# Kernel optimization log

Measured on AMD Instinct MI355X. Metric: run time of the kernel, lower is better.

The kernel has to match this reference:

```python
import jax, jax.numpy as jnp
import numpy as np

B, L, D, H, NE, M, NP, C, F2 = 2, 1024, 768, 12, 42, 8, 1722, 97, 256


def setup_inputs() -> dict:
    key = jax.random.key(0)
    ks = jax.random.split(key, 12)
    s = 0.02
    sequence_output = jax.random.normal(ks[0], (B, L, D), jnp.float32)
    attention = jax.random.uniform(ks[1], (B, H, L, L), jnp.float32)
    mention_idx = jax.random.randint(ks[2], (B, NE, M), 0, L)
    mention_mask = jax.random.randint(ks[3], (B, NE, M), 0, 2).at[:, :, 0].set(1)
    hts = jax.random.randint(ks[4], (B, NP, 2), 0, NE)
    return dict(
        sequence_output=sequence_output, attention=attention,
        mention_idx=mention_idx, mention_mask=mention_mask, hts=hts,
        W_lin=jax.random.normal(ks[5], (D, 3)) * s, b_lin=jnp.zeros((3,)),
        W_seg=jax.random.normal(ks[6], (3, F2)) * s, b_seg=jnp.zeros((F2,)),
        W_head=jax.random.normal(ks[7], (D, F2)) * s, b_head=jnp.zeros((F2,)),
        W_tail=jax.random.normal(ks[8], (D, F2)) * s, b_tail=jnp.zeros((F2,)),
        W_bil=jax.random.normal(ks[9], (C, F2, F2)) * s, b_bil=jnp.zeros((C,)),
    )


def reference(sequence_output, attention, mention_idx, mention_mask, hts,
              W_lin, b_lin, W_seg, b_seg, W_head, b_head, W_tail, b_tail,
              W_bil, b_bil):
    b_, l_, d_ = sequence_output.shape
    h_ = attention.shape[1]
    ne, m_ = mention_idx.shape[1:]
    NEG = jnp.asarray(-1e30, sequence_output.dtype)
    msk = mention_mask.astype(sequence_output.dtype)  # [B,NE,M]

    bidx = jnp.arange(b_)[:, None, None]
    # --- get_hrt: per-entity mention gather + logsumexp pool / mean pool ---
    ment_emb = sequence_output[bidx, mention_idx]              # [B,NE,M,D]
    ent_emb = jax.nn.logsumexp(jnp.where(msk[..., None] > 0, ment_emb, NEG), axis=2)  # [B,NE,D]
    ment_att = attention[bidx, :, mention_idx]                 # [B,NE,M,H,L]
    ent_att = (ment_att * msk[..., None, None]).sum(2) / msk.sum(2)[..., None, None]  # [B,NE,H,L]

    b2 = jnp.arange(b_)[:, None]
    hs = ent_emb[b2, hts[..., 0]]                              # [B,NP,D]
    ts = ent_emb[b2, hts[..., 1]]

    # --- get_channel_map: all ne*ne pair attention-weighted context ---
    hi = jnp.repeat(jnp.arange(ne), ne)
    ti = jnp.tile(jnp.arange(ne), ne)
    h_att = ent_att[:, hi]                                     # [B,NE*NE,H,L]
    t_att = ent_att[:, ti]
    ht_att = jnp.einsum('bphl,bphl->bpl', h_att, t_att) / h_   # mean over heads
    ht_att = ht_att / (ht_att.sum(-1, keepdims=True) + 1e-5)
    rs = jnp.einsum('bld,bpl->bpd', sequence_output, ht_att)   # [B,NE*NE,D]
    feature_map = rs.reshape(b_, ne, ne, d_)

    # self.linear (D->3) then segmentation net (stand-in: 1x1 conv 3->F2 + relu)
    attn_input = feature_map @ W_lin + b_lin                   # [B,NE,NE,3]
    attn_map = jax.nn.relu(attn_input @ W_seg + b_seg)         # [B,NE,NE,F2]

    # --- get_ht: gather pair features ---
    h_t = attn_map[b2, hts[..., 0], hts[..., 1]]               # [B,NP,F2]
    hs = jnp.tanh(hs @ W_head + b_head + h_t)
    ts = jnp.tanh(ts @ W_tail + b_tail + h_t)
    logits = jnp.einsum('bpi,oij,bpj->bpo', hs, W_bil, ts) + b_bil
    return logits.reshape(-1, logits.shape[-1])               # [B*NP, C]
```

## Files before the change

### kernel.cpp

```cpp
#include <hip/hip_runtime.h>
#include <hip/hip_bf16.h>
#include <math.h>

constexpr int BB = 2;
constexpr int LL = 1024;
constexpr int DD = 768;
constexpr int HH = 12;
constexpr int NEz = 42;
constexpr int MM = 8;
constexpr int NPp = 1722;
constexpr int CC = 97;
constexpr int FF = 256;
constexpr int PAIRS = NEz * NEz;
constexpr int TOTAL = BB * NPp;

constexpr int MT = 96;
constexpr int NT = 36;
constexpr int OG2 = 7;
constexpr int NOG = 14;
constexpr int NWG2 = NT * NOG;

typedef float f32x4 __attribute__((ext_vector_type(4)));
typedef short bf16x8 __attribute__((ext_vector_type(8)));
typedef unsigned short u16x4 __attribute__((ext_vector_type(4)));

__device__ inline short f2bs(float x) {
    __hip_bfloat16 b = __float2bfloat16(x);
    return *(short*)&b;
}
__device__ inline float bs2f(unsigned short u) {
    return __uint_as_float(((unsigned)u) << 16);
}
__device__ inline void gload16(const void* g, void* l) {
    __builtin_amdgcn_global_load_lds((const __attribute__((address_space(1))) unsigned int*)g,
                                     (__attribute__((address_space(3))) unsigned int*)l, 16, 0, 0);
}

__global__ void k_seqw(const float* __restrict__ seq, const float* __restrict__ Wl,
                       float* __restrict__ seqW) {
    int bl = blockIdx.x;
    int lane = threadIdx.x;
    const float* row = seq + (size_t)bl * DD;
    float a0 = 0.f, a1 = 0.f, a2 = 0.f;
    for (int d = lane; d < DD; d += 64) {
        float v = row[d];
        a0 += v * Wl[d * 3 + 0];
        a1 += v * Wl[d * 3 + 1];
        a2 += v * Wl[d * 3 + 2];
    }
    for (int off = 32; off; off >>= 1) {
        a0 += __shfl_down(a0, off);
        a1 += __shfl_down(a1, off);
        a2 += __shfl_down(a2, off);
    }
    if (lane == 0) {
        seqW[bl * 3 + 0] = a0;
        seqW[bl * 3 + 1] = a1;
        seqW[bl * 3 + 2] = a2;
    }
}

__global__ void k_ent_emb(const float* __restrict__ seq, const int* __restrict__ midx,
                          const int* __restrict__ mmask, float* __restrict__ ent_emb) {
    int be = blockIdx.x;
    int b = be / NEz;
    int tid = threadIdx.x;
    int idx[MM], msk[MM];
#pragma unroll
    for (int m = 0; m < MM; ++m) {
        idx[m] = midx[be * MM + m];
        msk[m] = mmask[be * MM + m];
    }
    const float* sb = seq + (size_t)b * LL * DD;
    for (int d = tid; d < DD; d += 256) {
        float v[MM];
        float mx = -1e30f;
#pragma unroll
        for (int m = 0; m < MM; ++m) {
            v[m] = msk[m] ? sb[(size_t)idx[m] * DD + d] : -1e30f;
            mx = fmaxf(mx, v[m]);
        }
        float s = 0.f;
#pragma unroll
        for (int m = 0; m < MM; ++m) s += expf(v[m] - mx);
        ent_emb[(size_t)be * DD + d] = mx + logf(s);
    }
}

__global__ void k_ent_att(const float* __restrict__ att, const int* __restrict__ midx,
                          const int* __restrict__ mmask, float* __restrict__ ea) {
    int beh = blockIdx.x;
    int h = beh % HH;
    int be = beh / HH;
    int b = be / NEz;
    int tid = threadIdx.x;
    int idx[MM], msk[MM];
    float msum = 0.f;
#pragma unroll
    for (int m = 0; m < MM; ++m) {
        idx[m] = midx[be * MM + m];
        msk[m] = mmask[be * MM + m];
        msum += (float)msk[m];
    }
    float inv = 1.f / msum;
    const float* ab = att + ((size_t)b * HH + h) * LL * LL;
#pragma unroll
    for (int li = 0; li < 4; ++li) {
        int l = tid + li * 256;
        float acc = 0.f;
#pragma unroll
        for (int m = 0; m < MM; ++m)
            if (msk[m]) acc += ab[(size_t)idx[m] * LL + l];
        ea[(size_t)beh * LL + l] = acc * inv;
    }
}

__global__ void k_pairAB(const float* __restrict__ ea, const float* __restrict__ seqW,
                         float* __restrict__ szp) {
    int lcb = blockIdx.x;
    int b = blockIdx.y;
    int l0 = lcb * 8;
    int tid = threadIdx.x;
    int lane = tid & 63;
    int e1 = (tid >> 6) * 8 + (lane >> 3);
    int l = lane & 7;

    __shared__ float S[NEz][HH][9];
    __shared__ float sw[8][3];

    for (int idx = tid; idx < NEz * HH * 8; idx += 384) {
        int e = idx / 96, rem = idx % 96;
        int h = rem / 8, ll = rem % 8;
        S[e][h][ll] = ea[((size_t)(b * NEz + e) * HH + h) * LL + l0 + ll];
    }
    if (tid < 24) sw[tid / 3][tid % 3] = seqW[((size_t)b * LL + l0 + tid / 3) * 3 + tid % 3];
    __syncthreads();

    bool act = e1 < NEz;
    float e1r[HH];
#pragma unroll
    for (int h = 0; h < HH; ++h) e1r[h] = act ? S[e1][h][l] : 0.f;
    float sw0 = sw[l][0], sw1 = sw[l][1], sw2 = sw[l][2];

    for (int e2 = 0; e2 < NEz; ++e2) {
        float ht = 0.f;
#pragma unroll
        for (int h = 0; h < HH; ++h) ht += e1r[h] * S[e2][h][l];
        ht *= (1.0f / HH);
        float v0 = ht, v1 = ht * sw0, v2 = ht * sw1, v3 = ht * sw2;
#pragma unroll
        for (int off = 1; off < 8; off <<= 1) {
            v0 += __shfl_xor(v0, off);
            v1 += __shfl_xor(v1, off);
            v2 += __shfl_xor(v2, off);
            v3 += __shfl_xor(v3, off);
        }
        if (act && l == 0) {
            float4 o4 = make_float4(v0, v1, v2, v3);
            *(float4*)&szp[((size_t)(b * 128 + lcb) * PAIRS + e1 * NEz + e2) * 4] = o4;
        }
    }
}

__global__ void k_pairC(const float* __restrict__ szp, const float* __restrict__ Wseg,
                        const float* __restrict__ bseg, const float* __restrict__ blin,
                        float* __restrict__ am) {
    int bp = blockIdx.x;
    int b = bp / PAIRS;
    int p = bp % PAIRS;
    int tid = threadIdx.x;

    __shared__ float zz[3];
    if (tid < 64) {
        float4 a = *(const float4*)&szp[((size_t)(b * 128 + tid) * PAIRS + p) * 4];
        float4 c = *(const float4*)&szp[((size_t)(b * 128 + tid + 64) * PAIRS + p) * 4];
        float v0 = a.x + c.x, v1 = a.y + c.y, v2 = a.z + c.z, v3 = a.w + c.w;
#pragma unroll
        for (int off = 1; off < 64; off <<= 1) {
            v0 += __shfl_xor(v0, off);
            v1 += __shfl_xor(v1, off);
            v2 += __shfl_xor(v2, off);
            v3 += __shfl_xor(v3, off);
        }
        if (tid == 0) {
            float inv = 1.f / (v0 + 1e-5f);
            zz[0] = v1 * inv + blin[0];
            zz[1] = v2 * inv + blin[1];
            zz[2] = v3 * inv + blin[2];
        }
    }
    __syncthreads();
    float val = zz[0] * Wseg[tid] + zz[1] * Wseg[FF + tid] + zz[2] * Wseg[2 * FF + tid] + bseg[tid];
    am[(size_t)bp * FF + tid] = fmaxf(val, 0.f);
}

__global__ void k_ew(const float* __restrict__ ent_emb, const float* __restrict__ Wh,
                     const float* __restrict__ bh, const float* __restrict__ Wt,
                     const float* __restrict__ bt, float* __restrict__ EWh,
                     float* __restrict__ EWt) {
    int be = blockIdx.x;
    int tid = threadIdx.x;
    __shared__ float e[DD];
    for (int d = tid; d < DD; d += 256) e[d] = ent_emb[(size_t)be * DD + d];
    __syncthreads();
    float ah = bh[tid], at = bt[tid];
    for (int d = 0; d < DD; ++d) {
        float ev = e[d];
        ah += ev * Wh[d * FF + tid];
        at += ev * Wt[d * FF + tid];
    }
    EWh[(size_t)be * FF + tid] = ah;
    EWt[(size_t)be * FF + tid] = at;
}

__global__ void k_wt(const float* __restrict__ Wb, short* __restrict__ Wf) {
    int o = blockIdx.y;
    int kt = blockIdx.x >> 2, ct = blockIdx.x & 3;
    int tid = threadIdx.x;
    int lane6 = tid & 63, q = tid >> 6;
    __shared__ float t64[64][65];
    const float* src = Wb + (size_t)o * FF * FF;
#pragma unroll 4
    for (int i = 0; i < 16; ++i) {
        int kk = q * 16 + i;
        t64[kk][lane6] = src[(size_t)(kt * 64 + kk) * FF + ct * 64 + lane6];
    }
    __syncthreads();
    int kr = kt >> 1, wc = ct;
#pragma unroll
    for (int s = 0; s < 2; ++s) {
        int slot = tid + s * 256;
        int ks2 = slot >> 8, ni = (slot >> 6) & 3, ln = slot & 63;
        int kl = ks2 * 32 + (ln >> 4) * 8;
        int nl = ni * 16 + (ln & 15);
        bf16x8 val;
#pragma unroll
        for (int j = 0; j < 8; ++j) val[j] = f2bs(t64[kl + j][nl]);
        int ksg = (kt & 1) * 2 + ks2;
        size_t off = ((((size_t)(o * 2 + kr) * 4 + wc) * 4 + ksg) * 4 + ni) * 64 + ln;
        *(bf16x8*)(Wf + off * 8) = val;
    }
}

__global__ void k_prep(const float* __restrict__ EWh, const float* __restrict__ EWt,
                       const float* __restrict__ am, const int* __restrict__ hts,
                       short* __restrict__ HSf, short* __restrict__ TSt) {
    int tile = blockIdx.x;
    int tid = threadIdx.x;
    for (int s = tid; s < 3072; s += 512) {
        int ln = s & 63, kc = (s >> 6) & 3;
        int mk = s >> 8;
        int mi = mk % 6, kr = mk / 6;
        int p = tile * MT + mi * 16 + (ln & 15);
        int k = kr * 128 + kc * 32 + (ln >> 4) * 8;
        bf16x8 v = {0, 0, 0, 0, 0, 0, 0, 0};
        if (p < TOTAL) {
            int b = p / NPp;
            int e1 = hts[p * 2 + 0], e2 = hts[p * 2 + 1];
            const float* hr = EWh + (size_t)(b * NEz + e1) * FF + k;
            const float* ar = am + ((size_t)b * PAIRS + e1 * NEz + e2) * FF + k;
#pragma unroll
            for (int j = 0; j < 8; ++j) v[j] = f2bs(tanhf(hr[j] + ar[j]));
        }
        size_t off = ((size_t)tile * 48 + kr * 24 + mi * 4 + kc) * 64 + ln;
        *(bf16x8*)(HSf + off * 8) = v;
    }
    for (int idx = tid; idx < FF * MT; idx += 512) {
        int c = idx / MT, r = idx % MT;
        int p = tile * MT + r;
        short v = 0;
        if (p < TOTAL) {
            int b = p / NPp;
            int e1 = hts[p * 2 + 0], e2 = hts[p * 2 + 1];
            float a = am[((size_t)b * PAIRS + e1 * NEz + e2) * FF + c];
            v = f2bs(tanhf(EWt[(size_t)(b * NEz + e2) * FF + c] + a));
        }
        TSt[(size_t)tile * 25600 + c * 100 + r] = v;
    }
}

__launch_bounds__(512, 2)
__global__ void k_bil(const short* __restrict__ HSf, const short* __restrict__ TSt,
                      const short* __restrict__ Wf, const float* __restrict__ bbil,
                      float* __restrict__ out) {
    int f = blockIdx.x;
    int wg = (f & 7) * 63 + (f >> 3);
    int og = wg / NT;
    int tile = wg % NT;
    int o0 = og * OG2;
    int nO = (CC - o0 < OG2) ? (CC - o0) : OG2;

    int tid = threadIdx.x;
    int lane = tid & 63, w = tid >> 6;
    int kr = w >> 2, wc = w & 3;
    int lr = lane & 15, lg = lane >> 4;

    __shared__ short TSl[FF * 100];
    __shared__ float red[OG2][MT][8];
    __shared__ char Bbuf[8][8192];

    {
        const unsigned int* ts_src = (const unsigned int*)(TSt + (size_t)tile * 25600);
        unsigned int* ts_dst = (unsigned int*)TSl;
        for (int i = tid; i < 12800; i += 512) ts_dst[i] = ts_src[i];
    }

    bf16x8 af[6][4];
    {
        const short* ab = HSf + ((size_t)tile * 48 + kr * 24) * 512;
#pragma unroll
        for (int mi = 0; mi < 6; ++mi)
#pragma unroll
            for (int kc = 0; kc < 4; ++kc)
                af[mi][kc] = *(const bf16x8*)(ab + ((mi * 4 + kc) * 64 + lane) * 8);
    }

    char* Bw = &Bbuf[w][0];
    const char* Wfb = (const char*)Wf + (size_t)(kr * 4 + wc) * 16384;

    {
        const char* s = Wfb + (size_t)o0 * 131072;
#pragma unroll
        for (int fi = 0; fi < 4; ++fi)
            gload16(s + fi * 1024 + lane * 16, Bw + fi * 1024 + lane * 16);
    }
    __syncthreads();

    for (int oi = 0; oi < nO; ++oi) {
        f32x4 acc[6][4];
#pragma unroll
        for (int mi = 0; mi < 6; ++mi)
#pragma unroll
            for (int ni = 0; ni < 4; ++ni) acc[mi][ni] = (f32x4){0.f, 0.f, 0.f, 0.f};

#pragma unroll
        for (int kc = 0; kc < 4; ++kc) {
            asm volatile("s_waitcnt vmcnt(0)" ::: "memory");
            __builtin_amdgcn_sched_barrier(0);
            bf16x8 bfr[4];
#pragma unroll
            for (int ni = 0; ni < 4; ++ni)
                bfr[ni] = *(const bf16x8*)(Bw + (kc & 1) * 4096 + ni * 1024 + lane * 16);
            __builtin_amdgcn_sched_barrier(0);
            {
                int cc1 = oi * 4 + kc + 1;
                if (cc1 < nO * 4) {
                    const char* s = Wfb + (size_t)(o0 + (cc1 >> 2)) * 131072 + (cc1 & 3) * 4096;
                    char* d = Bw + ((kc + 1) & 1) * 4096;
#pragma unroll
                    for (int fi = 0; fi < 4; ++fi)
                        gload16(s + fi * 1024 + lane * 16, d + fi * 1024 + lane * 16);
                }
            }
            __builtin_amdgcn_sched_barrier(0);
            __builtin_amdgcn_s_setprio(1);
#pragma unroll
            for (int ni = 0; ni < 4; ++ni)
#pragma unroll
                for (int mi = 0; mi < 6; ++mi)
                    acc[mi][ni] = __builtin_amdgcn_mfma_f32_16x16x32_bf16(
                        af[mi][kc], bfr[ni], acc[mi][ni], 0, 0, 0);
            __builtin_amdgcn_s_setprio(0);
        }

#pragma unroll
        for (int mi = 0; mi < 6; ++mi) {
            int rb = mi * 16 + lg * 4;
            float sum[4] = {0.f, 0.f, 0.f, 0.f};
#pragma unroll
            for (int ni = 0; ni < 4; ++ni) {
                int c = wc * 64 + ni * 16 + lr;
                u16x4 ts4 = *(const u16x4*)(TSl + c * 100 + rb);
#pragma unroll
                for (int reg = 0; reg < 4; ++reg)
                    sum[reg] += acc[mi][ni][reg] * bs2f(ts4[reg]);
            }
#pragma unroll
            for (int reg = 0; reg < 4; ++reg) {
                float v = sum[reg];
                v += __shfl_xor(v, 1);
                v += __shfl_xor(v, 2);
                v += __shfl_xor(v, 4);
                v += __shfl_xor(v, 8);
                if (lr == 0) red[oi][rb + reg][w] = v;
            }
        }
    }

    __syncthreads();
    for (int t = tid; t < nO * MT; t += 512) {
        int oi = t / MT, r = t % MT;
        int p = tile * MT + r;
        if (p < TOTAL) {
            float s = red[oi][r][0] + red[oi][r][1] + red[oi][r][2] + red[oi][r][3] +
                      red[oi][r][4] + red[oi][r][5] + red[oi][r][6] + red[oi][r][7];
            out[(size_t)p * CC + o0 + oi] = s + bbil[o0 + oi];
        }
    }
}

extern "C" void kernel_launch(void* const* d_in, const int* in_sizes, int n_in,
                              void* d_out, int out_size, void* d_ws, size_t ws_size,
                              hipStream_t stream) {
    const float* seq   = (const float*)d_in[0];
    const float* att   = (const float*)d_in[1];
    const int*   midx  = (const int*)d_in[2];
    const int*   mmask = (const int*)d_in[3];
    const int*   hts   = (const int*)d_in[4];
    const float* Wlin  = (const float*)d_in[5];
    const float* blin  = (const float*)d_in[6];
    const float* Wseg  = (const float*)d_in[7];
    const float* bseg  = (const float*)d_in[8];
    const float* Whead = (const float*)d_in[9];
    const float* bhead = (const float*)d_in[10];
    const float* Wtail = (const float*)d_in[11];
    const float* btail = (const float*)d_in[12];
    const float* Wbil  = (const float*)d_in[13];
    const float* bbil  = (const float*)d_in[14];
    float* out = (float*)d_out;

    float* ws = (float*)d_ws;
    float* ent_emb = ws;
    float* ea      = ent_emb + BB * NEz * DD;
    float* seqW    = ea + (size_t)BB * NEz * HH * LL;
    float* EWh     = seqW + BB * LL * 3;
    float* EWt     = EWh + BB * NEz * FF;
    float* am      = EWt + BB * NEz * FF;
    float* szp     = am + (size_t)BB * PAIRS * FF;
    short* Wf      = (short*)(szp + (size_t)BB * 128 * PAIRS * 4);
    short* HSf     = Wf + (size_t)CC * FF * FF;
    short* TSt     = HSf + (size_t)NT * MT * FF;

    k_seqw<<<BB * LL, 64, 0, stream>>>(seq, Wlin, seqW);
    k_ent_emb<<<BB * NEz, 256, 0, stream>>>(seq, midx, mmask, ent_emb);
    k_ent_att<<<BB * NEz * HH, 256, 0, stream>>>(att, midx, mmask, ea);
    k_pairAB<<<dim3(128, BB), 384, 0, stream>>>(ea, seqW, szp);
    k_pairC<<<BB * PAIRS, 256, 0, stream>>>(szp, Wseg, bseg, blin, am);
    k_ew<<<BB * NEz, 256, 0, stream>>>(ent_emb, Whead, bhead, Wtail, btail, EWh, EWt);
    k_wt<<<dim3(16, CC), 256, 0, stream>>>(Wbil, Wf);
    k_prep<<<NT, 512, 0, stream>>>(EWh, EWt, am, hts, HSf, TSt);
    k_bil<<<NWG2, 512, 0, stream>>>(HSf, TSt, Wf, bbil, out);
}
```

Before: 235.1 us.

## Restructure bilinear GEMM into double-buffered swizzled tiles and fuse pair pipeline

The bilinear kernel now uses 256-row M tiles over the full K=256 with A and B both staged into double-buffered, XOR-swizzled LDS via global_load_lds. Each workgroup processes 2-3 output classes strided across the grid, and the tail-side contraction reads TS directly from global memory. Elsewhere, the seq·W_lin projection is fused into k_pairAB, k_pairC is replaced by a small zz reduction with the segmentation ReLU recomputed inside k_prep, and the k_ew and k_wt layouts are reorganised. This cuts launches and the large attn_map intermediate, at the cost of redundant recomputation in prep and higher LDS pressure in the GEMM.

```diff
diff --git a/kernel.cpp b/kernel.cpp
--- a/kernel.cpp
+++ b/kernel.cpp
@@ -13,51 +13,23 @@
 constexpr int FF = 256;
 constexpr int PAIRS = NEz * NEz;
 constexpr int TOTAL = BB * NPp;
-
-constexpr int MT = 96;
-constexpr int NT = 36;
-constexpr int OG2 = 7;
-constexpr int NOG = 14;
-constexpr int NWG2 = NT * NOG;
+constexpr int MTv = 256;
+constexpr int NTt = 14;
+constexpr int PADR = 3584;
+constexpr int NOGv = 36;
+constexpr int NWGv = NTt * NOGv;
 
 typedef float f32x4 __attribute__((ext_vector_type(4)));
 typedef short bf16x8 __attribute__((ext_vector_type(8)));
-typedef unsigned short u16x4 __attribute__((ext_vector_type(4)));
+typedef unsigned int u32x2 __attribute__((ext_vector_type(2)));
 
 __device__ inline short f2bs(float x) {
     __hip_bfloat16 b = __float2bfloat16(x);
     return *(short*)&b;
 }
-__device__ inline float bs2f(unsigned short u) {
-    return __uint_as_float(((unsigned)u) << 16);
-}
 __device__ inline void gload16(const void* g, void* l) {
     __builtin_amdgcn_global_load_lds((const __attribute__((address_space(1))) unsigned int*)g,
                                      (__attribute__((address_space(3))) unsigned int*)l, 16, 0, 0);
-}
-
-__global__ void k_seqw(const float* __restrict__ seq, const float* __restrict__ Wl,
-                       float* __restrict__ seqW) {
-    int bl = blockIdx.x;
-    int lane = threadIdx.x;
-    const float* row = seq + (size_t)bl * DD;
-    float a0 = 0.f, a1 = 0.f, a2 = 0.f;
-    for (int d = lane; d < DD; d += 64) {
-        float v = row[d];
-        a0 += v * Wl[d * 3 + 0];
-        a1 += v * Wl[d * 3 + 1];
-        a2 += v * Wl[d * 3 + 2];
-    }
-    for (int off = 32; off; off >>= 1) {
-        a0 += __shfl_down(a0, off);
-        a1 += __shfl_down(a1, off);
-        a2 += __shfl_down(a2, off);
-    }
-    if (lane == 0) {
-        seqW[bl * 3 + 0] = a0;
-        seqW[bl * 3 + 1] = a1;
-        seqW[bl * 3 + 2] = a2;
-    }
 }
 
 __global__ void k_ent_emb(const float* __restrict__ seq, const int* __restrict__ midx,
@@ -115,8 +87,8 @@
     }
 }
 
-__global__ void k_pairAB(const float* __restrict__ ea, const float* __restrict__ seqW,
-                         float* __restrict__ szp) {
+__global__ void k_pairAB(const float* __restrict__ ea, const float* __restrict__ seq,
+                         const float* __restrict__ Wl, float* __restrict__ szp) {
     int lcb = blockIdx.x;
     int b = blockIdx.y;
     int l0 = lcb * 8;
@@ -127,13 +99,30 @@
 
     __shared__ float S[NEz][HH][9];
     __shared__ float sw[8][3];
+    __shared__ float swp[24][17];
 
     for (int idx = tid; idx < NEz * HH * 8; idx += 384) {
         int e = idx / 96, rem = idx % 96;
         int h = rem / 8, ll = rem % 8;
         S[e][h][ll] = ea[((size_t)(b * NEz + e) * HH + h) * LL + l0 + ll];
     }
-    if (tid < 24) sw[tid / 3][tid % 3] = seqW[((size_t)b * LL + l0 + tid / 3) * 3 + tid % 3];
+    {
+        int cpair = tid % 24, s = tid / 24;
+        if (s < 16) {
+            int ll = cpair / 3, kk = cpair % 3;
+            const float* sr = seq + ((size_t)b * LL + l0 + ll) * DD;
+            float p = 0.f;
+            for (int d = s * 48; d < s * 48 + 48; ++d) p += sr[d] * Wl[d * 3 + kk];
+            swp[cpair][s] = p;
+        }
+    }
+    __syncthreads();
+    if (tid < 24) {
+        float s = 0.f;
+#pragma unroll
+        for (int i = 0; i < 16; ++i) s += swp[tid][i];
+        sw[tid / 3][tid % 3] = s;
+    }
     __syncthreads();
 
     bool act = e1 < NEz;
@@ -157,247 +146,286 @@
         }
         if (act && l == 0) {
             float4 o4 = make_float4(v0, v1, v2, v3);
-            *(float4*)&szp[((size_t)(b * 128 + lcb) * PAIRS + e1 * NEz + e2) * 4] = o4;
-        }
-    }
-}
-
-__global__ void k_pairC(const float* __restrict__ szp, const float* __restrict__ Wseg,
-                        const float* __restrict__ bseg, const float* __restrict__ blin,
-                        float* __restrict__ am) {
-    int bp = blockIdx.x;
-    int b = bp / PAIRS;
-    int p = bp % PAIRS;
-    int tid = threadIdx.x;
-
-    __shared__ float zz[3];
-    if (tid < 64) {
-        float4 a = *(const float4*)&szp[((size_t)(b * 128 + tid) * PAIRS + p) * 4];
-        float4 c = *(const float4*)&szp[((size_t)(b * 128 + tid + 64) * PAIRS + p) * 4];
-        float v0 = a.x + c.x, v1 = a.y + c.y, v2 = a.z + c.z, v3 = a.w + c.w;
-#pragma unroll
-        for (int off = 1; off < 64; off <<= 1) {
-            v0 += __shfl_xor(v0, off);
-            v1 += __shfl_xor(v1, off);
-            v2 += __shfl_xor(v2, off);
-            v3 += __shfl_xor(v3, off);
-        }
-        if (tid == 0) {
-            float inv = 1.f / (v0 + 1e-5f);
-            zz[0] = v1 * inv + blin[0];
-            zz[1] = v2 * inv + blin[1];
-            zz[2] = v3 * inv + blin[2];
-        }
-    }
-    __syncthreads();
-    float val = zz[0] * Wseg[tid] + zz[1] * Wseg[FF + tid] + zz[2] * Wseg[2 * FF + tid] + bseg[tid];
-    am[(size_t)bp * FF + tid] = fmaxf(val, 0.f);
+            *(float4*)&szp[(((size_t)(b * PAIRS + e1 * NEz + e2)) * 128 + lcb) * 4] = o4;
+        }
+    }
+}
+
+__global__ void k_zz(const float* __restrict__ szp, const float* __restrict__ blin,
+                     float* __restrict__ zz) {
+    int bp = blockIdx.x * 256 + threadIdx.x;
+    if (bp >= BB * PAIRS) return;
+    const float4* s = (const float4*)(szp + (size_t)bp * 512);
+    float v0 = 0.f, v1 = 0.f, v2 = 0.f, v3 = 0.f;
+#pragma unroll 8
+    for (int i = 0; i < 128; ++i) {
+        float4 a = s[i];
+        v0 += a.x; v1 += a.y; v2 += a.z; v3 += a.w;
+    }
+    float inv = 1.f / (v0 + 1e-5f);
+    float4 o4 = make_float4(v1 * inv + blin[0], v2 * inv + blin[1], v3 * inv + blin[2], 0.f);
+    *(float4*)&zz[(size_t)bp * 4] = o4;
 }
 
 __global__ void k_ew(const float* __restrict__ ent_emb, const float* __restrict__ Wh,
                      const float* __restrict__ bh, const float* __restrict__ Wt,
                      const float* __restrict__ bt, float* __restrict__ EWh,
                      float* __restrict__ EWt) {
-    int be = blockIdx.x;
-    int tid = threadIdx.x;
-    __shared__ float e[DD];
-    for (int d = tid; d < DD; d += 256) e[d] = ent_emb[(size_t)be * DD + d];
+    int cb = blockIdx.x;
+    int tid = threadIdx.x;
+    int colg = cb * 8 + (tid & 7);
+    int rg = tid >> 3;
+    bool head = colg < FF;
+    int col = head ? colg : colg - FF;
+    const float* W = head ? Wh : Wt;
+    float bias = head ? bh[col] : bt[col];
+    float* dst = head ? EWh : EWt;
+    for (int r = rg; r < BB * NEz; r += 32) {
+        float s = bias;
+        const float* e = ent_emb + (size_t)r * DD;
+        for (int d = 0; d < DD; ++d) s += e[d] * W[(size_t)d * FF + col];
+        dst[(size_t)r * FF + col] = s;
+    }
+}
+
+__global__ void k_wt(const float* __restrict__ Wb, char* __restrict__ Wf) {
+    int o = blockIdx.x >> 2, kc = blockIdx.x & 3;
+    int tid = threadIdx.x;
+    __shared__ float t64[64][257];
+    const float* src = Wb + (size_t)o * FF * FF + (size_t)(kc * 64) * FF;
+#pragma unroll
+    for (int i = 0; i < 64; ++i) {
+        int flat = i * 256 + tid;
+        t64[flat >> 8][flat & 255] = src[flat];
+    }
     __syncthreads();
-    float ah = bh[tid], at = bt[tid];
-    for (int d = 0; d < DD; ++d) {
-        float ev = e[d];
-        ah += ev * Wh[d * FF + tid];
-        at += ev * Wt[d * FF + tid];
-    }
-    EWh[(size_t)be * FF + tid] = ah;
-    EWt[(size_t)be * FF + tid] = at;
-}
-
-__global__ void k_wt(const float* __restrict__ Wb, short* __restrict__ Wf) {
-    int o = blockIdx.y;
-    int kt = blockIdx.x >> 2, ct = blockIdx.x & 3;
-    int tid = threadIdx.x;
-    int lane6 = tid & 63, q = tid >> 6;
-    __shared__ float t64[64][65];
-    const float* src = Wb + (size_t)o * FF * FF;
-#pragma unroll 4
-    for (int i = 0; i < 16; ++i) {
-        int kk = q * 16 + i;
-        t64[kk][lane6] = src[(size_t)(kt * 64 + kk) * FF + ct * 64 + lane6];
-    }
-    __syncthreads();
-    int kr = kt >> 1, wc = ct;
-#pragma unroll
-    for (int s = 0; s < 2; ++s) {
-        int slot = tid + s * 256;
-        int ks2 = slot >> 8, ni = (slot >> 6) & 3, ln = slot & 63;
-        int kl = ks2 * 32 + (ln >> 4) * 8;
-        int nl = ni * 16 + (ln & 15);
-        bf16x8 val;
-#pragma unroll
-        for (int j = 0; j < 8; ++j) val[j] = f2bs(t64[kl + j][nl]);
-        int ksg = (kt & 1) * 2 + ks2;
-        size_t off = ((((size_t)(o * 2 + kr) * 4 + wc) * 4 + ksg) * 4 + ni) * 64 + ln;
-        *(bf16x8*)(Wf + off * 8) = val;
+    char* dst = Wf + ((size_t)o * 4 + kc) * 32768;
+#pragma unroll
+    for (int i = 0; i < 8; ++i) {
+        int u = i * 256 + tid;
+        int c = u >> 3, k16 = u & 7;
+        bf16x8 v;
+#pragma unroll
+        for (int j = 0; j < 8; ++j) v[j] = f2bs(t64[k16 * 8 + j][c]);
+        *(bf16x8*)(dst + ((c * 128 + k16 * 16) ^ ((c & 7) << 4))) = v;
     }
 }
 
 __global__ void k_prep(const float* __restrict__ EWh, const float* __restrict__ EWt,
-                       const float* __restrict__ am, const int* __restrict__ hts,
-                       short* __restrict__ HSf, short* __restrict__ TSt) {
-    int tile = blockIdx.x;
-    int tid = threadIdx.x;
-    for (int s = tid; s < 3072; s += 512) {
-        int ln = s & 63, kc = (s >> 6) & 3;
-        int mk = s >> 8;
-        int mi = mk % 6, kr = mk / 6;
-        int p = tile * MT + mi * 16 + (ln & 15);
-        int k = kr * 128 + kc * 32 + (ln >> 4) * 8;
-        bf16x8 v = {0, 0, 0, 0, 0, 0, 0, 0};
+                       const float* __restrict__ zz, const float* __restrict__ Wseg,
+                       const float* __restrict__ bseg, const int* __restrict__ hts,
+                       char* __restrict__ HSf, unsigned short* __restrict__ TSt) {
+    int bx = blockIdx.x;
+    int mt = bx >> 2, cs = bx & 3;
+    int tid = threadIdx.x;
+    int p0 = mt * MTv;
+
+    __shared__ int offh[256], offt[256];
+    __shared__ float zr[256][4];
+    __shared__ float wsg[4][64];
+    {
+        int p = p0 + tid;
         if (p < TOTAL) {
             int b = p / NPp;
-            int e1 = hts[p * 2 + 0], e2 = hts[p * 2 + 1];
-            const float* hr = EWh + (size_t)(b * NEz + e1) * FF + k;
-            const float* ar = am + ((size_t)b * PAIRS + e1 * NEz + e2) * FF + k;
-#pragma unroll
-            for (int j = 0; j < 8; ++j) v[j] = f2bs(tanhf(hr[j] + ar[j]));
-        }
-        size_t off = ((size_t)tile * 48 + kr * 24 + mi * 4 + kc) * 64 + ln;
-        *(bf16x8*)(HSf + off * 8) = v;
-    }
-    for (int idx = tid; idx < FF * MT; idx += 512) {
-        int c = idx / MT, r = idx % MT;
-        int p = tile * MT + r;
-        short v = 0;
-        if (p < TOTAL) {
-            int b = p / NPp;
-            int e1 = hts[p * 2 + 0], e2 = hts[p * 2 + 1];
-            float a = am[((size_t)b * PAIRS + e1 * NEz + e2) * FF + c];
-            v = f2bs(tanhf(EWt[(size_t)(b * NEz + e2) * FF + c] + a));
-        }
-        TSt[(size_t)tile * 25600 + c * 100 + r] = v;
-    }
-}
+            int e1 = hts[p * 2], e2 = hts[p * 2 + 1];
+            offh[tid] = (b * NEz + e1) * FF;
+            offt[tid] = (b * NEz + e2) * FF;
+            float4 z4 = *(const float4*)(zz + (size_t)(b * PAIRS + e1 * NEz + e2) * 4);
+            zr[tid][0] = z4.x; zr[tid][1] = z4.y; zr[tid][2] = z4.z; zr[tid][3] = 0.f;
+        } else {
+            offh[tid] = -1; offt[tid] = -1;
+            zr[tid][0] = zr[tid][1] = zr[tid][2] = zr[tid][3] = 0.f;
+        }
+        if (tid < 64) {
+            int c = cs * 64 + tid;
+            wsg[0][tid] = Wseg[c];
+            wsg[1][tid] = Wseg[FF + c];
+            wsg[2][tid] = Wseg[2 * FF + c];
+            wsg[3][tid] = bseg[c];
+        }
+    }
+    __syncthreads();
+
+    char* dst = HSf + ((size_t)mt * 4 + cs) * 32768;
+#pragma unroll
+    for (int i = 0; i < 8; ++i) {
+        int u = i * 256 + tid;
+        int r = u >> 3, k8 = u & 7;
+        int oh = offh[r];
+        bf16x8 v = {0, 0, 0, 0, 0, 0, 0, 0};
+        if (oh >= 0) {
+#pragma unroll
+            for (int j = 0; j < 8; ++j) {
+                int cl = k8 * 8 + j;
+                float ht = fmaxf(zr[r][0] * wsg[0][cl] + zr[r][1] * wsg[1][cl] +
+                                 zr[r][2] * wsg[2][cl] + wsg[3][cl], 0.f);
+                v[j] = f2bs(tanhf(EWh[oh + cs * 64 + cl] + ht));
+            }
+        }
+        *(bf16x8*)(dst + ((r * 128 + k8 * 16) ^ ((r & 7) << 4))) = v;
+    }
+#pragma unroll
+    for (int i = 0; i < 64; ++i) {
+        int u = i * 256 + tid;
+        int r = u & 255, cl = u >> 8;
+        int c = cs * 64 + cl;
+        int ot = offt[r];
+        unsigned short v = 0;
+        if (ot >= 0) {
+            float ht = fmaxf(zr[r][0] * wsg[0][cl] + zr[r][1] * wsg[1][cl] +
+                             zr[r][2] * wsg[2][cl] + wsg[3][cl], 0.f);
+            v = (unsigned short)f2bs(tanhf(EWt[ot + c] + ht));
+        }
+        TSt[(size_t)c * PADR + p0 + r] = v;
+    }
+}
+
+#define STAGE(TT, BUF) do { \
+    int kc_ = (TT) & 3; \
+    int o_ = og + NOGv * ((TT) >> 2); \
+    const char* As_ = HSf + ((size_t)(mt * 4 + kc_)) * 32768; \
+    const char* Bs_ = Wf + ((size_t)(o_ * 4 + kc_)) * 32768; \
+    _Pragma("unroll") \
+    for (int i_ = 0; i_ < 4; ++i_) { \
+        gload16(As_ + (i_ * 512 + tid) * 16, Ab[BUF] + (i_ * 512 + tid) * 16); \
+        gload16(Bs_ + (i_ * 512 + tid) * 16, Bb[BUF] + (i_ * 512 + tid) * 16); \
+    } \
+} while (0)
 
 __launch_bounds__(512, 2)
-__global__ void k_bil(const short* __restrict__ HSf, const short* __restrict__ TSt,
-                      const short* __restrict__ Wf, const float* __restrict__ bbil,
+__global__ void k_bil(const char* __restrict__ HSf, const unsigned short* __restrict__ TSt,
+                      const char* __restrict__ Wf, const float* __restrict__ bbil,
                       float* __restrict__ out) {
     int f = blockIdx.x;
     int wg = (f & 7) * 63 + (f >> 3);
-    int og = wg / NT;
-    int tile = wg % NT;
-    int o0 = og * OG2;
-    int nO = (CC - o0 < OG2) ? (CC - o0) : OG2;
+    int og = wg / NTt;
+    int mt = wg % NTt;
+    int p0 = mt * MTv;
+    int nO = (og < 25) ? 3 : 2;
 
     int tid = threadIdx.x;
     int lane = tid & 63, w = tid >> 6;
-    int kr = w >> 2, wc = w & 3;
+    int wr = w >> 2, wc = w & 3;
     int lr = lane & 15, lg = lane >> 4;
-
-    __shared__ short TSl[FF * 100];
-    __shared__ float red[OG2][MT][8];
-    __shared__ char Bbuf[8][8192];
-
-    {
-        const unsigned int* ts_src = (const unsigned int*)(TSt + (size_t)tile * 25600);
-        unsigned int* ts_dst = (unsigned int*)TSl;
-        for (int i = tid; i < 12800; i += 512) ts_dst[i] = ts_src[i];
-    }
-
-    bf16x8 af[6][4];
-    {
-        const short* ab = HSf + ((size_t)tile * 48 + kr * 24) * 512;
-#pragma unroll
-        for (int mi = 0; mi < 6; ++mi)
-#pragma unroll
-            for (int kc = 0; kc < 4; ++kc)
-                af[mi][kc] = *(const bf16x8*)(ab + ((mi * 4 + kc) * 64 + lane) * 8);
-    }
-
-    char* Bw = &Bbuf[w][0];
-    const char* Wfb = (const char*)Wf + (size_t)(kr * 4 + wc) * 16384;
-
-    {
-        const char* s = Wfb + (size_t)o0 * 131072;
-#pragma unroll
-        for (int fi = 0; fi < 4; ++fi)
-            gload16(s + fi * 1024 + lane * 16, Bw + fi * 1024 + lane * 16);
-    }
-    __syncthreads();
-
-    for (int oi = 0; oi < nO; ++oi) {
-        f32x4 acc[6][4];
-#pragma unroll
-        for (int mi = 0; mi < 6; ++mi)
-#pragma unroll
-            for (int ni = 0; ni < 4; ++ni) acc[mi][ni] = (f32x4){0.f, 0.f, 0.f, 0.f};
-
-#pragma unroll
-        for (int kc = 0; kc < 4; ++kc) {
-            asm volatile("s_waitcnt vmcnt(0)" ::: "memory");
-            __builtin_amdgcn_sched_barrier(0);
-            bf16x8 bfr[4];
+    int swz = (lr & 7) << 4;
+
+    __shared__ char Ab[2][32768];
+    __shared__ char Bb[2][32768];
+    __shared__ float red[MTv][4];
+
+    STAGE(0, 0);
+    STAGE(1, 1);
+
+    f32x4 acc[8][4];
+#pragma unroll
+    for (int mi = 0; mi < 8; ++mi)
+#pragma unroll
+        for (int ni = 0; ni < 4; ++ni) acc[mi][ni] = (f32x4){0.f, 0.f, 0.f, 0.f};
+
+    int T = 4 * nO;
+    for (int t = 0; t < T; ++t) {
+        int cur = t & 1;
+        __builtin_amdgcn_sched_barrier(0);
+        asm volatile("s_waitcnt vmcnt(8)" ::: "memory");
+        __builtin_amdgcn_sched_barrier(0);
+        __builtin_amdgcn_s_barrier();
+        __builtin_amdgcn_sched_barrier(0);
+
+        const char* Ac = Ab[cur];
+        const char* Bc = Bb[cur];
+        int kA = (lg * 16) ^ swz;
+        int kB = (64 + lg * 16) ^ swz;
+
+        bf16x8 a0[8], b0[4];
+#pragma unroll
+        for (int mi = 0; mi < 8; ++mi)
+            a0[mi] = *(const bf16x8*)(Ac + (wr * 128 + mi * 16 + lr) * 128 + kA);
+#pragma unroll
+        for (int ni = 0; ni < 4; ++ni)
+            b0[ni] = *(const bf16x8*)(Bc + (wc * 64 + ni * 16 + lr) * 128 + kA);
+        __builtin_amdgcn_s_setprio(1);
+#pragma unroll
+        for (int mi = 0; mi < 8; ++mi)
 #pragma unroll
             for (int ni = 0; ni < 4; ++ni)
-                bfr[ni] = *(const bf16x8*)(Bw + (kc & 1) * 4096 + ni * 1024 + lane * 16);
-            __builtin_amdgcn_sched_barrier(0);
-            {
-                int cc1 = oi * 4 + kc + 1;
-                if (cc1 < nO * 4) {
-                    const char* s = Wfb + (size_t)(o0 + (cc1 >> 2)) * 131072 + (cc1 & 3) * 4096;
-                    char* d = Bw + ((kc + 1) & 1) * 4096;
-#pragma unroll
-                    for (int fi = 0; fi < 4; ++fi)
-                        gload16(s + fi * 1024 + lane * 16, d + fi * 1024 + lane * 16);
+                acc[mi][ni] = __builtin_amdgcn_mfma_f32_16x16x32_bf16(a0[mi], b0[ni], acc[mi][ni], 0, 0, 0);
+        __builtin_amdgcn_s_setprio(0);
+
+        bf16x8 a1[8], b1[4];
+#pragma unroll
+        for (int mi = 0; mi < 8; ++mi)
+            a1[mi] = *(const bf16x8*)(Ac + (wr * 128 + mi * 16 + lr) * 128 + kB);
+#pragma unroll
+        for (int ni = 0; ni < 4; ++ni)
+            b1[ni] = *(const bf16x8*)(Bc + (wc * 64 + ni * 16 + lr) * 128 + kB);
+        __builtin_amdgcn_sched_barrier(0);
+        asm volatile("s_waitcnt lgkmcnt(0)" ::: "memory");
+        __builtin_amdgcn_sched_barrier(0);
+        __builtin_amdgcn_s_barrier();
+        __builtin_amdgcn_sched_barrier(0);
+
+        int tt = (t + 2 < T) ? t + 2 : T - 1;
+        STAGE(tt, cur);
+        __builtin_amdgcn_sched_barrier(0);
+        __builtin_amdgcn_s_setprio(1);
+#pragma unroll
+        for (int mi = 0; mi < 8; ++mi)
+#pragma unroll
+            for (int ni = 0; ni < 4; ++ni)
+                acc[mi][ni] = __builtin_amdgcn_mfma_f32_16x16x32_bf16(a1[mi], b1[ni], acc[mi][ni], 0, 0, 0);
+        __builtin_amdgcn_s_setprio(0);
+
+        if ((t & 3) == 3) {
+            int o = og + NOGv * (t >> 2);
+            u32x2 tsv[8][4];
+#pragma unroll
+            for (int mi = 0; mi < 8; ++mi)
+#pragma unroll
+                for (int ni = 0; ni < 4; ++ni)
+                    tsv[mi][ni] = *(const u32x2*)(TSt + (size_t)(wc * 64 + ni * 16 + lr) * PADR +
+                                                  p0 + wr * 128 + mi * 16 + lg * 4);
+#pragma unroll
+            for (int mi = 0; mi < 8; ++mi) {
+                float s0 = 0.f, s1 = 0.f, s2 = 0.f, s3 = 0.f;
+#pragma unroll
+                for (int ni = 0; ni < 4; ++ni) {
+                    unsigned lo = tsv[mi][ni][0], hi = tsv[mi][ni][1];
+                    s0 += acc[mi][ni][0] * __uint_as_float(lo << 16);
+                    s1 += acc[mi][ni][1] * __uint_as_float(lo & 0xFFFF0000u);
+                    s2 += acc[mi][ni][2] * __uint_as_float(hi << 16);
+                    s3 += acc[mi][ni][3] * __uint_as_float(hi & 0xFFFF0000u);
+                    acc[mi][ni] = (f32x4){0.f, 0.f, 0.f, 0.f};
+                }
+#pragma unroll
+                for (int off = 1; off < 16; off <<= 1) {
+                    s0 += __shfl_xor(s0, off);
+                    s1 += __shfl_xor(s1, off);
+                    s2 += __shfl_xor(s2, off);
+                    s3 += __shfl_xor(s3, off);
+                }
+                if (lr == 0) {
+                    int rb = wr * 128 + mi * 16 + lg * 4;
+                    red[rb + 0][wc] = s0;
+                    red[rb + 1][wc] = s1;
+                    red[rb + 2][wc] = s2;
+                    red[rb + 3][wc] = s3;
                 }
             }
             __builtin_amdgcn_sched_barrier(0);
-            __builtin_amdgcn_s_setprio(1);
-#pragma unroll
-            for (int ni = 0; ni < 4; ++ni)
-#pragma unroll
-                for (int mi = 0; mi < 6; ++mi)
-                    acc[mi][ni] = __builtin_amdgcn_mfma_f32_16x16x32_bf16(
-                        af[mi][kc], bfr[ni], acc[mi][ni], 0, 0, 0);
-            __builtin_amdgcn_s_setprio(0);
-        }
-
-#pragma unroll
-        for (int mi = 0; mi < 6; ++mi) {
-            int rb = mi * 16 + lg * 4;
-            float sum[4] = {0.f, 0.f, 0.f, 0.f};
-#pragma unroll
-            for (int ni = 0; ni < 4; ++ni) {
-                int c = wc * 64 + ni * 16 + lr;
-                u16x4 ts4 = *(const u16x4*)(TSl + c * 100 + rb);
-#pragma unroll
-                for (int reg = 0; reg < 4; ++reg)
-                    sum[reg] += acc[mi][ni][reg] * bs2f(ts4[reg]);
+            asm volatile("s_waitcnt lgkmcnt(0)" ::: "memory");
+            __builtin_amdgcn_sched_barrier(0);
+            __builtin_amdgcn_s_barrier();
+            __builtin_amdgcn_sched_barrier(0);
+            if (tid < 256) {
+                int p = p0 + tid;
+                if (p < TOTAL)
+                    out[(size_t)p * CC + o] =
+                        red[tid][0] + red[tid][1] + red[tid][2] + red[tid][3] + bbil[o];
             }
-#pragma unroll
-            for (int reg = 0; reg < 4; ++reg) {
-                float v = sum[reg];
-                v += __shfl_xor(v, 1);
-                v += __shfl_xor(v, 2);
-                v += __shfl_xor(v, 4);
-                v += __shfl_xor(v, 8);
-                if (lr == 0) red[oi][rb + reg][w] = v;
-            }
-        }
-    }
-
-    __syncthreads();
-    for (int t = tid; t < nO * MT; t += 512) {
-        int oi = t / MT, r = t % MT;
-        int p = tile * MT + r;
-        if (p < TOTAL) {
-            float s = red[oi][r][0] + red[oi][r][1] + red[oi][r][2] + red[oi][r][3] +
-                      red[oi][r][4] + red[oi][r][5] + red[oi][r][6] + red[oi][r][7];
-            out[(size_t)p * CC + o0 + oi] = s + bbil[o0 + oi];
-        }
-    }
-}
+        }
+    }
+}
+#undef STAGE
 
 extern "C" void kernel_launch(void* const* d_in, const int* in_sizes, int n_in,
                               void* d_out, int out_size, void* d_ws, size_t ws_size,
@@ -422,22 +450,20 @@
     float* ws = (float*)d_ws;
     float* ent_emb = ws;
     float* ea      = ent_emb + BB * NEz * DD;
-    float* seqW    = ea + (size_t)BB * NEz * HH * LL;
-    float* EWh     = seqW + BB * LL * 3;
+    float* szp     = ea + (size_t)BB * NEz * HH * LL;
+    float* zz      = szp + (size_t)BB * PAIRS * 128 * 4;
+    float* EWh     = zz + (size_t)BB * PAIRS * 4;
     float* EWt     = EWh + BB * NEz * FF;
-    float* am      = EWt + BB * NEz * FF;
-    float* szp     = am + (size_t)BB * PAIRS * FF;
-    short* Wf      = (short*)(szp + (size_t)BB * 128 * PAIRS * 4);
-    short* HSf     = Wf + (size_t)CC * FF * FF;
-    short* TSt     = HSf + (size_t)NT * MT * FF;
-
-    k_seqw<<<BB * LL, 64, 0, stream>>>(seq, Wlin, seqW);
+    char* Wf       = (char*)(EWt + BB * NEz * FF);
+    char* HSf      = Wf + (size_t)CC * 4 * 32768;
+    unsigned short* TSt = (unsigned short*)(HSf + (size_t)NTt * 4 * 32768);
+
     k_ent_emb<<<BB * NEz, 256, 0, stream>>>(seq, midx, mmask, ent_emb);
     k_ent_att<<<BB * NEz * HH, 256, 0, stream>>>(att, midx, mmask, ea);
-    k_pairAB<<<dim3(128, BB), 384, 0, stream>>>(ea, seqW, szp);
-    k_pairC<<<BB * PAIRS, 256, 0, stream>>>(szp, Wseg, bseg, blin, am);
-    k_ew<<<BB * NEz, 256, 0, stream>>>(ent_emb, Whead, bhead, Wtail, btail, EWh, EWt);
-    k_wt<<<dim3(16, CC), 256, 0, stream>>>(Wbil, Wf);
-    k_prep<<<NT, 512, 0, stream>>>(EWh, EWt, am, hts, HSf, TSt);
-    k_bil<<<NWG2, 512, 0, stream>>>(HSf, TSt, Wf, bbil, out);
-}
+    k_pairAB<<<dim3(128, BB), 384, 0, stream>>>(ea, seq, Wlin, szp);
+    k_zz<<<14, 256, 0, stream>>>(szp, blin, zz);
+    k_ew<<<64, 256, 0, stream>>>(ent_emb, Whead, bhead, Wtail, btail, EWh, EWt);
+    k_wt<<<CC * 4, 256, 0, stream>>>(Wbil, Wf);
+    k_prep<<<NTt * 4, 256, 0, stream>>>(EWh, EWt, zz, Wseg, bseg, hts, HSf, TSt);
+    k_bil<<<NWGv, 512, 0, stream>>>(HSf, TSt, Wf, bbil, out);
+}
```

Measured after the change: 239.5 us. About the same (+1.9%).
